# Optimization experiments

Measured on AMD Instinct MI355X. Metric: run time of the kernel, lower is better.

The kernel has to match this reference:

```python
import jax, jax.numpy as jnp
import numpy as np

B, N, E_PER_G = 32, 2048, 16384
NF, NHID, NCLS = 128, 128, 10
RATIO = 0.5
NT = B * N
E = B * E_PER_G
K1 = int(np.ceil(RATIO * N))        # 1024 nodes kept per graph after pool1
K2 = int(np.ceil(RATIO * K1))       # 512
K3 = int(np.ceil(RATIO * K2))       # 256


def setup_inputs() -> dict:
    key = jax.random.key(0)
    ks = jax.random.split(key, 16)
    x = jax.random.normal(ks[0], (NT, NF), dtype=jnp.float32)
    off = (jnp.arange(B, dtype=jnp.int32) * N)[:, None]
    src = (jax.random.randint(ks[1], (B, E_PER_G), 0, N, dtype=jnp.int32) + off).reshape(-1)
    dst = (jax.random.randint(ks[2], (B, E_PER_G), 0, N, dtype=jnp.int32) + off).reshape(-1)
    edge_index = jnp.stack([src, dst])
    batch = jnp.repeat(jnp.arange(B, dtype=jnp.int32), N)
    def lin(k, i, o):
        return jax.random.normal(k, (i, o), jnp.float32) / np.float32(np.sqrt(i))
    return {
        'x': x, 'edge_index': edge_index, 'batch': batch,
        'W1': lin(ks[3], NF, NHID), 'b1': jnp.zeros((NHID,), jnp.float32),
        'Wp1': lin(ks[4], NHID, 1), 'bp1': jnp.zeros((1,), jnp.float32),
        'W2': lin(ks[5], NHID, NHID), 'b2': jnp.zeros((NHID,), jnp.float32),
        'Wp2': lin(ks[6], NHID, 1), 'bp2': jnp.zeros((1,), jnp.float32),
        'W3': lin(ks[7], NHID, NHID), 'b3': jnp.zeros((NHID,), jnp.float32),
        'Wp3': lin(ks[8], NHID, 1), 'bp3': jnp.zeros((1,), jnp.float32),
        'lin1_W': lin(ks[9], 2 * NHID, NHID), 'lin1_b': jnp.zeros((NHID,), jnp.float32),
        'lin2_W': lin(ks[10], NHID, NHID // 2), 'lin2_b': jnp.zeros((NHID // 2,), jnp.float32),
        'lin3_W': lin(ks[11], NHID // 2, NCLS), 'lin3_b': jnp.zeros((NCLS,), jnp.float32),
    }


def gcn(x, src, dst, emask, nmask, W, b):
    # PyG GCNConv: add self-loops, symmetric normalization D^-1/2 (A+I) D^-1/2 @ (x W) + b.
    # Removed nodes/edges carry weight 0 via masks (equivalent to filter_adj re-indexing).
    h = x @ W
    deg = jnp.zeros((NT,), h.dtype).at[dst].add(emask) + nmask
    dinv = jnp.where(deg > 0, 1.0, 0.0) * jax.lax.rsqrt(jnp.where(deg > 0, deg, 1.0))
    coef = dinv[src] * dinv[dst] * emask               # [E]
    out = jnp.zeros_like(h).at[dst].add(coef[:, None] * h[src])
    out = out + ((dinv * dinv) * nmask)[:, None] * h   # self-loop term, norm = 1/deg
    return out + b


def sagpool(x, src, dst, emask, nmask, Wp, bp, k):
    # score = GCNConv(nhid,1); keep top-k per graph; x <- x[perm] * tanh(score[perm])
    score = gcn(x, src, dst, emask, nmask, Wp, bp)[:, 0]          # [NT]
    s = jnp.where(nmask > 0, score, -jnp.inf).reshape(B, N)
    _, idx = jax.lax.top_k(s, k)                                   # [B, k]
    keep = jnp.zeros((B, N), x.dtype).at[jnp.arange(B)[:, None], idx].set(1.0).reshape(-1)
    x_new = x * jnp.tanh(score)[:, None] * keep[:, None]
    emask_new = emask * keep[src] * keep[dst]                      # filter_adj
    return x_new, emask_new, keep


def readout(x, nmask, count):
    # [global_max_pool, global_mean_pool] over active nodes of each graph
    xb = x.reshape(B, N, -1)
    m = nmask.reshape(B, N, 1)
    mx = jnp.max(jnp.where(m > 0, xb, -jnp.inf), axis=1)
    mn = jnp.sum(xb * m, axis=1) / count
    return jnp.concatenate([mx, mn], axis=-1)


def reference(x, edge_index, batch, W1, b1, Wp1, bp1, W2, b2, Wp2, bp2,
              W3, b3, Wp3, bp3, lin1_W, lin1_b, lin2_W, lin2_b, lin3_W, lin3_b):
    src, dst = edge_index[0], edge_index[1]
    emask = jnp.ones((E,), x.dtype)
    nmask = jnp.ones((NT,), x.dtype)

    h = jax.nn.relu(gcn(x, src, dst, emask, nmask, W1, b1))
    h, emask, nmask = sagpool(h, src, dst, emask, nmask, Wp1, bp1, K1)
    x1 = readout(h, nmask, jnp.asarray(K1, x.dtype))

    h = jax.nn.relu(gcn(h, src, dst, emask, nmask, W2, b2))
    h, emask, nmask = sagpool(h, src, dst, emask, nmask, Wp2, bp2, K2)
    x2 = readout(h, nmask, jnp.asarray(K2, x.dtype))

    h = jax.nn.relu(gcn(h, src, dst, emask, nmask, W3, b3))
    h, emask, nmask = sagpool(h, src, dst, emask, nmask, Wp3, bp3, K3)
    x3 = readout(h, nmask, jnp.asarray(K3, x.dtype))

    g = x1 + x2 + x3
    g = jax.nn.relu(g @ lin1_W + lin1_b)   # dropout = identity in eval
    g = jax.nn.relu(g @ lin2_W + lin2_b)
    return jax.nn.log_softmax(g @ lin3_W + lin3_b, axis=-1)
```

## Files before the change

kernel.cpp:

```cpp
#include <hip/hip_runtime.h>
#include <math.h>


namespace {

constexpr int B_  = 32;
constexpr int N_  = 2048;
constexpr int NT  = B_ * N_;
constexpr int EPG = 16384;
constexpr int E_  = B_ * EPG;
constexpr int NCLS = 10;
constexpr int AST = 132;

__device__ __forceinline__ int relabel(int bpgsh) {
  int x = blockIdx.x & 7, slot = blockIdx.x >> 3;
  int g = x + 8 * (slot >> bpgsh);
  return (g << bpgsh) + (slot & ((1 << bpgsh) - 1));
}

__global__ __launch_bounds__(1024) void k_csr(const int* __restrict__ src,
                                              const int* __restrict__ dst,
                                              int* __restrict__ off,
                                              int* __restrict__ srcp,
                                              float* __restrict__ dinv,
                                              float* __restrict__ ds,
                                              float* __restrict__ sws) {
  __shared__ int hist[2048];
  __shared__ int wsum[16];
  const int g = blockIdx.x;
  const int t = threadIdx.x;
  const int base_n = g * N_;
  const int base_e = g * EPG;
  hist[t] = 0;
  hist[t + 1024] = 0;
  __syncthreads();
#pragma unroll
  for (int i = 0; i < EPG / 1024; ++i) {
    int d = dst[base_e + t + 1024 * i];
    atomicAdd(&hist[d - base_n], 1);
  }
  __syncthreads();
  int a0 = hist[2 * t], a1 = hist[2 * t + 1];
  int ps = a0 + a1;
  {
    int lane = t & 63, w = t >> 6;
    int v = ps;
#pragma unroll
    for (int o = 1; o < 64; o <<= 1) {
      int nv = __shfl_up(v, o);
      if (lane >= o) v += nv;
    }
    if (lane == 63) wsum[w] = v;
    __syncthreads();
    if (t == 0) {
      int accv = 0;
      for (int i = 0; i < 16; ++i) { int tmp = wsum[i]; wsum[i] = accv; accv += tmp; }
    }
    __syncthreads();
    int excl = wsum[w] + v - ps;
    off[base_n + 2 * t] = base_e + excl;
    off[base_n + 2 * t + 1] = base_e + excl + a0;
    hist[2 * t] = excl;
    hist[2 * t + 1] = excl + a0;
    float d0 = 1.f + (float)a0, d1 = 1.f + (float)a1;
    float di0 = 1.f / sqrtf(d0), di1 = 1.f / sqrtf(d1);
    dinv[base_n + 2 * t] = di0;
    dinv[base_n + 2 * t + 1] = di1;
    ds[base_n + 2 * t] = di0;
    ds[base_n + 2 * t + 1] = di1;
    sws[base_n + 2 * t] = di0 * di0;
    sws[base_n + 2 * t + 1] = di1 * di1;
    if (g == B_ - 1 && t == 0) off[NT] = E_;
  }
  __syncthreads();
#pragma unroll
  for (int i = 0; i < EPG / 1024; ++i) {
    int e = base_e + t + 1024 * i;
    int d = dst[e];
    int s = src[e];
    int slot = atomicAdd(&hist[d - base_n], 1);
    srcp[base_e + slot] = s;
  }
}

__global__ __launch_bounds__(256) void k_matmul(const float* __restrict__ A,
                                                const float* __restrict__ W,
                                                float* __restrict__ C,
                                                const int* __restrict__ kept,
                                                int kshift, int bpgsh,
                                                const float* __restrict__ scaleArr,
                                                float* __restrict__ pmx,
                                                float* __restrict__ psm) {
  __shared__ float Ast[2][32 * AST];
  __shared__ float Ws[2][32 * 128];
  __shared__ int rowid[128];
  __shared__ float rsc[128];
  const int tid = threadIdx.x;
  const int tile = relabel(bpgsh);
  if (kept) {
    if (tid < 128) {
      int q = tile * 128 + tid;
      int g = q >> kshift;
      int row = kept[g * N_ + (q - (g << kshift))];
      rowid[tid] = row;
      rsc[tid] = scaleArr[row];
    }
    __syncthreads();
  }
  const int rowq = tid >> 4;
  const int colq = tid & 15;
  float4 va[4], vw[4];
#pragma unroll
  for (int i = 0; i < 4; ++i) {
    int idx = tid + 256 * i;
    int row = idx & 127, fq = idx >> 7;
    int gr = kept ? rowid[row] : tile * 128 + row;
    va[i] = *(const float4*)&A[(size_t)gr * 128 + 4 * fq];
  }
#pragma unroll
  for (int i = 0; i < 4; ++i) {
    int idx = tid + 256 * i;
    int kk = idx >> 5, cf = idx & 31;
    vw[i] = *(const float4*)&W[(size_t)kk * 128 + 4 * cf];
  }
#pragma unroll
  for (int i = 0; i < 4; ++i) {
    int idx = tid + 256 * i;
    int row = idx & 127, fq = idx >> 7;
    Ast[0][(4 * fq + 0) * AST + row] = va[i].x;
    Ast[0][(4 * fq + 1) * AST + row] = va[i].y;
    Ast[0][(4 * fq + 2) * AST + row] = va[i].z;
    Ast[0][(4 * fq + 3) * AST + row] = va[i].w;
  }
#pragma unroll
  for (int i = 0; i < 4; ++i) {
    int idx = tid + 256 * i;
    int kk = idx >> 5, cf = idx & 31;
    *(float4*)&Ws[0][kk * 128 + 4 * cf] = vw[i];
  }
  __syncthreads();
  float acc[8][8] = {};
  for (int c = 0; c < 4; ++c) {
    int cur = c & 1;
    if (c < 3) {
      int k0n = 32 * (c + 1);
#pragma unroll
      for (int i = 0; i < 4; ++i) {
        int idx = tid + 256 * i;
        int row = idx & 127, fq = idx >> 7;
        int gr = kept ? rowid[row] : tile * 128 + row;
        va[i] = *(const float4*)&A[(size_t)gr * 128 + k0n + 4 * fq];
      }
#pragma unroll
      for (int i = 0; i < 4; ++i) {
        int idx = tid + 256 * i;
        int kk = idx >> 5, cf = idx & 31;
        vw[i] = *(const float4*)&W[(size_t)(k0n + kk) * 128 + 4 * cf];
      }
    }
#pragma unroll 2
    for (int kk = 0; kk < 32; ++kk) {
      float4 a0 = *(const float4*)&Ast[cur][kk * AST + 8 * rowq];
      float4 a1 = *(const float4*)&Ast[cur][kk * AST + 8 * rowq + 4];
      float4 w0 = *(const float4*)&Ws[cur][kk * 128 + 4 * colq];
      float4 w1 = *(const float4*)&Ws[cur][kk * 128 + 64 + 4 * colq];
      float a[8] = {a0.x, a0.y, a0.z, a0.w, a1.x, a1.y, a1.z, a1.w};
      float w[8] = {w0.x, w0.y, w0.z, w0.w, w1.x, w1.y, w1.z, w1.w};
#pragma unroll
      for (int r = 0; r < 8; ++r)
#pragma unroll
        for (int cc = 0; cc < 8; ++cc) acc[r][cc] += a[r] * w[cc];
    }
    if (kept) {
      int kkf = tid >> 3;
      int r0 = (tid & 7) * 16;
      float mxv = -INFINITY, smv = 0.f;
#pragma unroll
      for (int rr = 0; rr < 16; rr += 4) {
        float4 av = *(const float4*)&Ast[cur][kkf * AST + r0 + rr];
        float4 s4 = *(const float4*)&rsc[r0 + rr];
        float v0 = av.x * s4.x, v1 = av.y * s4.y;
        float v2 = av.z * s4.z, v3 = av.w * s4.w;
        mxv = fmaxf(fmaxf(fmaxf(mxv, v0), fmaxf(v1, v2)), v3);
        smv += v0 + v1 + v2 + v3;
      }
#pragma unroll
      for (int o = 4; o >= 1; o >>= 1) {
        mxv = fmaxf(mxv, __shfl_down(mxv, o));
        smv += __shfl_down(smv, o);
      }
      if ((tid & 7) == 0) {
        pmx[(size_t)tile * 128 + 32 * c + kkf] = mxv;
        psm[(size_t)tile * 128 + 32 * c + kkf] = smv;
      }
    }
    if (c < 3) {
      int nxt = cur ^ 1;
#pragma unroll
      for (int i = 0; i < 4; ++i) {
        int idx = tid + 256 * i;
        int row = idx & 127, fq = idx >> 7;
        Ast[nxt][(4 * fq + 0) * AST + row] = va[i].x;
        Ast[nxt][(4 * fq + 1) * AST + row] = va[i].y;
        Ast[nxt][(4 * fq + 2) * AST + row] = va[i].z;
        Ast[nxt][(4 * fq + 3) * AST + row] = va[i].w;
      }
#pragma unroll
      for (int i = 0; i < 4; ++i) {
        int idx = tid + 256 * i;
        int kk = idx >> 5, cf = idx & 31;
        *(float4*)&Ws[nxt][kk * 128 + 4 * cf] = vw[i];
      }
      __syncthreads();
    }
  }
#pragma unroll
  for (int r = 0; r < 8; ++r) {
    int gr = kept ? rowid[8 * rowq + r] : tile * 128 + 8 * rowq + r;
    float* Crow = &C[(size_t)gr * 128];
    *(float4*)&Crow[4 * colq] = make_float4(acc[r][0], acc[r][1], acc[r][2], acc[r][3]);
    *(float4*)&Crow[64 + 4 * colq] = make_float4(acc[r][4], acc[r][5], acc[r][6], acc[r][7]);
  }
}

__global__ __launch_bounds__(256) void k_agg(const float4* __restrict__ t4,
                                             const int* __restrict__ off,
                                             const int* __restrict__ srcp,
                                             const float* __restrict__ dinv,
                                             const float* __restrict__ ds,
                                             const float* __restrict__ sws,
                                             const float* __restrict__ bias,
                                             const float* __restrict__ Wp,
                                             float4* __restrict__ h4,
                                             float* __restrict__ t1,
                                             const int* __restrict__ kept,
                                             int kshift, int bpgsh) {
  int q = relabel(bpgsh) * 8 + (threadIdx.x >> 5);
  int node;
  if (kept) {
    int g = q >> kshift;
    node = kept[g * N_ + (q - (g << kshift))];
  } else {
    node = q;
  }
  const int lane = threadIdx.x & 31;
  const float dvi = dinv[node];
  float sw = sws[node];
  float4 self = t4[(size_t)node * 32 + lane];
  float4 acc = make_float4(sw * self.x, sw * self.y, sw * self.z, sw * self.w);
  int s = off[node], en = off[node + 1];
  int j = s;
  for (; j + 8 <= en; j += 8) {
    int sv[8];
    float cv[8];
#pragma unroll
    for (int i = 0; i < 8; ++i) sv[i] = srcp[j + i];
#pragma unroll
    for (int i = 0; i < 8; ++i) cv[i] = ds[sv[i]] * dvi;
#pragma unroll
    for (int i = 0; i < 8; ++i) {
      if (cv[i] != 0.f) {
        float4 r = t4[(size_t)sv[i] * 32 + lane];
        acc.x += cv[i] * r.x; acc.y += cv[i] * r.y;
        acc.z += cv[i] * r.z; acc.w += cv[i] * r.w;
      }
    }
  }
  for (; j < en; ++j) {
    int s0 = srcp[j];
    float c0 = ds[s0] * dvi;
    if (c0 != 0.f) {
      float4 r0 = t4[(size_t)s0 * 32 + lane];
      acc.x += c0 * r0.x; acc.y += c0 * r0.y; acc.z += c0 * r0.z; acc.w += c0 * r0.w;
    }
  }
  float4 b4 = ((const float4*)bias)[lane];
  acc.x = fmaxf(acc.x + b4.x, 0.f);
  acc.y = fmaxf(acc.y + b4.y, 0.f);
  acc.z = fmaxf(acc.z + b4.z, 0.f);
  acc.w = fmaxf(acc.w + b4.w, 0.f);
  h4[(size_t)node * 32 + lane] = acc;
  float4 wp = ((const float4*)Wp)[lane];
  float part = acc.x * wp.x + acc.y * wp.y + acc.z * wp.z + acc.w * wp.w;
#pragma unroll
  for (int o = 16; o > 0; o >>= 1) part += __shfl_down(part, o, 32);
  if (lane == 0) t1[node] = part;
}

__global__ __launch_bounds__(1024) void k_pool(const float* __restrict__ t1,
                                               const int* __restrict__ off,
                                               const int* __restrict__ srcp,
                                               float* __restrict__ dinv,
                                               float* __restrict__ ds,
                                               float* __restrict__ sws,
                                               float* __restrict__ scale,
                                               const float* __restrict__ bp,
                                               int* __restrict__ kept,
                                               const float4* __restrict__ h4,
                                               float* __restrict__ gout,
                                               float invk, int k) {
  __shared__ float st1[2048];
  __shared__ float sdv[2048];
  __shared__ float skp[2048];
  __shared__ int skept[1024];
  __shared__ unsigned rephist[4096];
  __shared__ unsigned ebits[64];
  __shared__ int wsum[16];
  __shared__ unsigned bc_digit, bc_prev;
  const int g = (blockIdx.x & 7) + 8 * (blockIdx.x >> 3);
  const int t = threadIdx.x;
  const int base = g * N_;
  st1[t] = t1[base + t];
  st1[t + 1024] = t1[base + t + 1024];
  sdv[t] = dinv[base + t];
  sdv[t + 1024] = dinv[base + t + 1024];
  if (t < 64) ebits[t] = 0u;
#pragma unroll
  for (int i = 0; i < 4; ++i) rephist[t + 1024 * i] = 0u;
  __syncthreads();
  float raw[2];
  unsigned key[2];
  float bpv = bp[0];
#pragma unroll
  for (int q = 0; q < 2; ++q) {
    int n = t + q * 1024;
    float di = sdv[n];
    float a = 0.f;
    int s = off[base + n], en = off[base + n + 1];
    int j = s;
    for (; j + 8 <= en; j += 8) {
      int sv[8];
#pragma unroll
      for (int i = 0; i < 8; ++i) sv[i] = srcp[j + i] - base;
#pragma unroll
      for (int i = 0; i < 8; ++i) a += sdv[sv[i]] * st1[sv[i]];
    }
    for (; j < en; ++j) {
      int sl = srcp[j] - base;
      a += sdv[sl] * st1[sl];
    }
    raw[q] = di * di * st1[n] + di * a + bpv;
    unsigned u = __float_as_uint(raw[q]);
    u = (u & 0x80000000u) ? ~u : (u | 0x80000000u);
    u = ~u;
    if (di <= 0.f) u = 0xFFFFFFFFu;
    key[q] = u;
  }
  unsigned prefix = 0u, rem = (unsigned)k;
  const int wv = t >> 6;
  for (int shift = 24; shift >= 0; shift -= 8) {
    unsigned mask = (shift == 24) ? 0u : (0xFFFFFFFFu << (shift + 8));
#pragma unroll
    for (int q = 0; q < 2; ++q)
      if ((key[q] & mask) == prefix)
        atomicAdd(&rephist[(wv << 8) + ((key[q] >> shift) & 255u)], 1u);
    __syncthreads();
    unsigned binv = 0u, v = 0u;
    if (t < 256) {
#pragma unroll
      for (int w = 0; w < 16; ++w) binv += rephist[(w << 8) + t];
      v = binv;
#pragma unroll
      for (int o = 1; o < 64; o <<= 1) {
        unsigned nv = __shfl_up(v, o);
        if ((t & 63) >= o) v += nv;
      }
      if ((t & 63) == 63) wsum[t >> 6] = (int)v;
    }
    __syncthreads();
    if (t < 256) {
      unsigned pre = 0u;
      int w4 = t >> 6;
      for (int u = 0; u < w4; ++u) pre += (unsigned)wsum[u];
      unsigned inc = v + pre, exc = inc - binv;
      if (inc >= rem && exc < rem) { bc_digit = (unsigned)t; bc_prev = exc; }
    }
    __syncthreads();
    if (shift > 0) {
#pragma unroll
      for (int i = 0; i < 4; ++i) rephist[t + 1024 * i] = 0u;
    }
    __syncthreads();
    prefix |= bc_digit << shift;
    rem -= bc_prev;
  }
  const unsigned Tkey = prefix;
  const int need = (int)rem;
#pragma unroll
  for (int q = 0; q < 2; ++q) {
    int n = t + q * 1024;
    if (key[q] == Tkey) atomicOr(&ebits[n >> 5], 1u << (n & 31));
  }
  __syncthreads();
#pragma unroll
  for (int q = 0; q < 2; ++q) {
    int n = t + q * 1024;
    float kp;
    if (key[q] < Tkey) {
      kp = 1.f;
    } else if (key[q] == Tkey) {
      int w = n >> 5;
      int rank = __popc(ebits[w] & ((1u << (n & 31)) - 1u));
      for (int u = 0; u < w; ++u) rank += __popc(ebits[u]);
      kp = (rank < need) ? 1.f : 0.f;
    } else {
      kp = 0.f;
    }
    skp[n] = kp;
    float sc = kp * tanhf(raw[q]);
    st1[n] = sc;
    scale[base + n] = sc;
  }
  __syncthreads();
  {
    int lane = t & 63, w = t >> 6;
    int a0 = (int)skp[2 * t], a1 = (int)skp[2 * t + 1];
    int ps = a0 + a1;
    int v = ps;
#pragma unroll
    for (int o = 1; o < 64; o <<= 1) {
      int nv = __shfl_up(v, o);
      if (lane >= o) v += nv;
    }
    if (lane == 63) wsum[w] = v;
    __syncthreads();
    if (t == 0) {
      int accv = 0;
      for (int i = 0; i < 16; ++i) { int tmp = wsum[i]; wsum[i] = accv; accv += tmp; }
    }
    __syncthreads();
    int excl = wsum[w] + v - ps;
    if (a0) { kept[base + excl] = base + 2 * t; skept[excl] = base + 2 * t; }
    if (a1) { kept[base + excl + a0] = base + 2 * t + 1; skept[excl + a0] = base + 2 * t + 1; }
  }
#pragma unroll
  for (int q = 0; q < 2; ++q) {
    int n = t + q * 1024;
    float nm = skp[n];
    float d = nm;
    int s = off[base + n], en = off[base + n + 1];
    int j = s;
    for (; j + 8 <= en; j += 8) {
      int sv[8];
#pragma unroll
      for (int i = 0; i < 8; ++i) sv[i] = srcp[j + i] - base;
#pragma unroll
      for (int i = 0; i < 8; ++i) d += skp[sv[i]];
    }
    for (; j < en; ++j) d += skp[srcp[j] - base];
    float di = (nm > 0.f) ? (1.f / sqrtf(d)) : 0.f;
    float sc = st1[n];
    dinv[base + n] = di;
    ds[base + n] = di * sc;
    sws[base + n] = di * di * sc;
  }
  if (!gout) return;
  __syncthreads();
  const int lane = t & 31, ng = t >> 5;
  float4 mx = make_float4(-INFINITY, -INFINITY, -INFINITY, -INFINITY);
  float4 sm = make_float4(0.f, 0.f, 0.f, 0.f);
  for (int i = ng; i < k; i += 32) {
    int node = skept[i];
    float sc = st1[node - base];
    float4 v = h4[(size_t)node * 32 + lane];
    v.x *= sc; v.y *= sc; v.z *= sc; v.w *= sc;
    mx.x = fmaxf(mx.x, v.x); mx.y = fmaxf(mx.y, v.y);
    mx.z = fmaxf(mx.z, v.z); mx.w = fmaxf(mx.w, v.w);
    sm.x += v.x; sm.y += v.y; sm.z += v.z; sm.w += v.w;
  }
  float4* red = (float4*)rephist;
  for (int d = 16; d >= 1; d >>= 1) {
    if (ng >= d && ng < 2 * d) {
      red[(ng - d) * 32 + lane] = mx;
      red[512 + (ng - d) * 32 + lane] = sm;
    }
    __syncthreads();
    if (ng < d) {
      float4 omx = red[ng * 32 + lane];
      float4 osm = red[512 + ng * 32 + lane];
      mx.x = fmaxf(mx.x, omx.x); mx.y = fmaxf(mx.y, omx.y);
      mx.z = fmaxf(mx.z, omx.z); mx.w = fmaxf(mx.w, omx.w);
      sm.x += osm.x; sm.y += osm.y; sm.z += osm.z; sm.w += osm.w;
    }
    __syncthreads();
  }
  if (ng == 0) {
    gout[g * 256 + 4 * lane + 0] = mx.x;
    gout[g * 256 + 4 * lane + 1] = mx.y;
    gout[g * 256 + 4 * lane + 2] = mx.z;
    gout[g * 256 + 4 * lane + 3] = mx.w;
    gout[g * 256 + 128 + 4 * lane + 0] = sm.x * invk;
    gout[g * 256 + 128 + 4 * lane + 1] = sm.y * invk;
    gout[g * 256 + 128 + 4 * lane + 2] = sm.z * invk;
    gout[g * 256 + 128 + 4 * lane + 3] = sm.w * invk;
  }
}

__global__ __launch_bounds__(128) void k_mlp(const float* __restrict__ pmxA,
                                             const float* __restrict__ psmA,
                                             const float* __restrict__ pmxB,
                                             const float* __restrict__ psmB,
                                             const float* __restrict__ goutC,
                                             const float* __restrict__ W1,
                                             const float* __restrict__ b1,
                                             const float* __restrict__ W2,
                                             const float* __restrict__ b2,
                                             const float* __restrict__ W3,
                                             const float* __restrict__ b3,
                                             float* __restrict__ out) {
  __shared__ float gr[256], o1[128], o2[64], o3[NCLS];
  int g = blockIdx.x, t = threadIdx.x;
  float mxA = -INFINITY, smA = 0.f;
#pragma unroll
  for (int p = 0; p < 8; ++p) {
    mxA = fmaxf(mxA, pmxA[(size_t)(g * 8 + p) * 128 + t]);
    smA += psmA[(size_t)(g * 8 + p) * 128 + t];
  }
  float mxB = -INFINITY, smB = 0.f;
#pragma unroll
  for (int p = 0; p < 4; ++p) {
    mxB = fmaxf(mxB, pmxB[(size_t)(g * 4 + p) * 128 + t]);
    smB += psmB[(size_t)(g * 4 + p) * 128 + t];
  }
  gr[t] = mxA + mxB + goutC[g * 256 + t];
  gr[t + 128] = smA * (1.f / 1024.f) + smB * (1.f / 512.f) + goutC[g * 256 + 128 + t];
  __syncthreads();
  float a = b1[t];
  for (int kk = 0; kk < 256; ++kk) a += gr[kk] * W1[kk * 128 + t];
  o1[t] = fmaxf(a, 0.f);
  __syncthreads();
  if (t < 64) {
    float a2 = b2[t];
    for (int kk = 0; kk < 128; ++kk) a2 += o1[kk] * W2[kk * 64 + t];
    o2[t] = fmaxf(a2, 0.f);
  }
  __syncthreads();
  if (t < NCLS) {
    float a3 = b3[t];
    for (int kk = 0; kk < 64; ++kk) a3 += o2[kk] * W3[kk * NCLS + t];
    o3[t] = a3;
  }
  __syncthreads();
  if (t == 0) {
    float m = -INFINITY;
    for (int c = 0; c < NCLS; ++c) m = fmaxf(m, o3[c]);
    float sum = 0.f;
    for (int c = 0; c < NCLS; ++c) sum += expf(o3[c] - m);
    float lse = logf(sum);
    for (int c = 0; c < NCLS; ++c) out[g * NCLS + c] = o3[c] - m - lse;
  }
}

}

extern "C" void kernel_launch(void* const* d_in, const int* in_sizes, int n_in,
                              void* d_out, int out_size, void* d_ws, size_t ws_size,
                              hipStream_t stream) {
  const float* x = (const float*)d_in[0];
  const int* ei = (const int*)d_in[1];
  const int* src = ei;
  const int* dst = ei + E_;
  const float* Wl[3]  = {(const float*)d_in[3], (const float*)d_in[7], (const float*)d_in[11]};
  const float* bl[3]  = {(const float*)d_in[4], (const float*)d_in[8], (const float*)d_in[12]};
  const float* Wpl[3] = {(const float*)d_in[5], (const float*)d_in[9], (const float*)d_in[13]};
  const float* bpl[3] = {(const float*)d_in[6], (const float*)d_in[10], (const float*)d_in[14]};
  const float* l1W = (const float*)d_in[15];
  const float* l1b = (const float*)d_in[16];
  const float* l2W = (const float*)d_in[17];
  const float* l2b = (const float*)d_in[18];
  const float* l3W = (const float*)d_in[19];
  const float* l3b = (const float*)d_in[20];

  char* p = (char*)d_ws;
  auto alloc = [&](size_t bytes) -> void* {
    void* r = (void*)p;
    p += (bytes + 255) & ~size_t(255);
    return r;
  };
  float* h      = (float*)alloc((size_t)NT * 128 * 4);
  float* t      = (float*)alloc((size_t)NT * 128 * 4);
  float* dinv   = (float*)alloc(NT * 4);
  float* ds     = (float*)alloc(NT * 4);
  float* sws    = (float*)alloc(NT * 4);
  float* scale  = (float*)alloc(NT * 4);
  float* t1     = (float*)alloc(NT * 4);
  int*   srcp   = (int*)alloc(E_ * 4);
  int*   off    = (int*)alloc((NT + 1) * 4);
  int*   kept0  = (int*)alloc(NT * 4);
  int*   kept1  = (int*)alloc(NT * 4);
  int*   kept2  = (int*)alloc(NT * 4);
  float* pmxA   = (float*)alloc(256 * 128 * 4);
  float* psmA   = (float*)alloc(256 * 128 * 4);
  float* pmxB   = (float*)alloc(128 * 128 * 4);
  float* psmB   = (float*)alloc(128 * 128 * 4);
  float* goutC  = (float*)alloc(B_ * 256 * 4);

  int* keptL[3] = {kept0, kept1, kept2};
  const int K[3] = {1024, 512, 256};
  const int KSH[3] = {10, 9, 8};
  float* pmxL[3] = {nullptr, pmxA, pmxB};
  float* psmL[3] = {nullptr, psmA, psmB};

  k_csr<<<B_, 1024, 0, stream>>>(src, dst, off, srcp, dinv, ds, sws);

  const float* inF = x;
  for (int l = 0; l < 3; ++l) {
    const int* inKept = (l == 0) ? nullptr : keptL[l - 1];
    int inKsh = (l == 0) ? 11 : KSH[l - 1];
    int nrows = (l == 0) ? NT : B_ * K[l - 1];
    int mm_bpgsh = (l == 0) ? 4 : (l == 1 ? 3 : 2);
    int ag_bpgsh = (l == 0) ? 8 : (l == 1 ? 7 : 6);
    k_matmul<<<nrows / 128, 256, 0, stream>>>(inF, Wl[l], t, inKept, inKsh, mm_bpgsh,
                                              scale, pmxL[l], psmL[l]);
    k_agg<<<nrows / 8, 256, 0, stream>>>((const float4*)t, off, srcp, dinv, ds, sws,
                                         bl[l], Wpl[l], (float4*)h, t1, inKept, inKsh,
                                         ag_bpgsh);
    k_pool<<<B_, 1024, 0, stream>>>(t1, off, srcp, dinv, ds, sws, scale, bpl[l],
                                    keptL[l], (const float4*)h,
                                    (l == 2) ? goutC : nullptr,
                                    1.f / (float)K[l], K[l]);
    inF = h;
  }
  k_mlp<<<B_, 128, 0, stream>>>(pmxA, psmA, pmxB, psmB, goutC,
                                l1W, l1b, l2W, l2b, l3W, l3b, (float*)d_out);
}
```

Measured before the change: 320.5 us.

## Fold CSR build into first matmul launch and MLP head into last pool

The CSR construction now runs in 32 extra blocks of the first matmul launch, reworked for 256-thread blocks with batched loads. The final MLP/log-softmax head is merged into the last k_pool kernel. k_pool also iterates only over the previously kept nodes instead of all 2048, and the matmul A-tile loads are remapped so consecutive threads read contiguous row segments. Together these remove two kernel launches and some redundant pool work. The costs are fewer threads for CSR building and a serial MLP tail inside the pool blocks.

```diff
diff --git a/kernel.cpp b/kernel.cpp
--- a/kernel.cpp
+++ b/kernel.cpp
@@ -12,74 +12,79 @@
 constexpr int NCLS = 10;
 constexpr int AST = 132;
 
-__device__ __forceinline__ int relabel(int bpgsh) {
-  int x = blockIdx.x & 7, slot = blockIdx.x >> 3;
+__device__ __forceinline__ int relabel(int bid, int bpgsh) {
+  int x = bid & 7, slot = bid >> 3;
   int g = x + 8 * (slot >> bpgsh);
   return (g << bpgsh) + (slot & ((1 << bpgsh) - 1));
 }
 
-__global__ __launch_bounds__(1024) void k_csr(const int* __restrict__ src,
-                                              const int* __restrict__ dst,
-                                              int* __restrict__ off,
-                                              int* __restrict__ srcp,
-                                              float* __restrict__ dinv,
-                                              float* __restrict__ ds,
-                                              float* __restrict__ sws) {
-  __shared__ int hist[2048];
-  __shared__ int wsum[16];
+__device__ void csr_build(const int* __restrict__ src, const int* __restrict__ dst,
+                          int* __restrict__ off, int* __restrict__ srcp,
+                          float* __restrict__ dinv, float* __restrict__ ds,
+                          float* __restrict__ sws, int* hist) {
   const int g = blockIdx.x;
   const int t = threadIdx.x;
   const int base_n = g * N_;
   const int base_e = g * EPG;
-  hist[t] = 0;
-  hist[t + 1024] = 0;
-  __syncthreads();
-#pragma unroll
-  for (int i = 0; i < EPG / 1024; ++i) {
-    int d = dst[base_e + t + 1024 * i];
-    atomicAdd(&hist[d - base_n], 1);
-  }
-  __syncthreads();
-  int a0 = hist[2 * t], a1 = hist[2 * t + 1];
-  int ps = a0 + a1;
+  int* wsum4 = hist + 2048;
+#pragma unroll
+  for (int i = 0; i < 8; ++i) hist[t + 256 * i] = 0;
+  __syncthreads();
+  for (int i = 0; i < EPG / 256; i += 8) {
+    int dd[8];
+#pragma unroll
+    for (int j = 0; j < 8; ++j) dd[j] = dst[base_e + t + 256 * (i + j)];
+#pragma unroll
+    for (int j = 0; j < 8; ++j) atomicAdd(&hist[dd[j] - base_n], 1);
+  }
+  __syncthreads();
+  int a[8], ssum = 0;
+#pragma unroll
+  for (int i = 0; i < 8; ++i) { a[i] = hist[8 * t + i]; ssum += a[i]; }
   {
     int lane = t & 63, w = t >> 6;
-    int v = ps;
+    int v = ssum;
 #pragma unroll
     for (int o = 1; o < 64; o <<= 1) {
       int nv = __shfl_up(v, o);
       if (lane >= o) v += nv;
     }
-    if (lane == 63) wsum[w] = v;
+    if (lane == 63) wsum4[w] = v;
     __syncthreads();
     if (t == 0) {
       int accv = 0;
-      for (int i = 0; i < 16; ++i) { int tmp = wsum[i]; wsum[i] = accv; accv += tmp; }
-    }
-    __syncthreads();
-    int excl = wsum[w] + v - ps;
-    off[base_n + 2 * t] = base_e + excl;
-    off[base_n + 2 * t + 1] = base_e + excl + a0;
-    hist[2 * t] = excl;
-    hist[2 * t + 1] = excl + a0;
-    float d0 = 1.f + (float)a0, d1 = 1.f + (float)a1;
-    float di0 = 1.f / sqrtf(d0), di1 = 1.f / sqrtf(d1);
-    dinv[base_n + 2 * t] = di0;
-    dinv[base_n + 2 * t + 1] = di1;
-    ds[base_n + 2 * t] = di0;
-    ds[base_n + 2 * t + 1] = di1;
-    sws[base_n + 2 * t] = di0 * di0;
-    sws[base_n + 2 * t + 1] = di1 * di1;
+      for (int i = 0; i < 4; ++i) { int tmp = wsum4[i]; wsum4[i] = accv; accv += tmp; }
+    }
+    __syncthreads();
+    int run = wsum4[w] + v - ssum;
+#pragma unroll
+    for (int i = 0; i < 8; ++i) {
+      int n = 8 * t + i;
+      off[base_n + n] = base_e + run;
+      hist[n] = run;
+      float d0 = 1.f + (float)a[i];
+      float di0 = 1.f / sqrtf(d0);
+      dinv[base_n + n] = di0;
+      ds[base_n + n] = di0;
+      sws[base_n + n] = di0 * di0;
+      run += a[i];
+    }
     if (g == B_ - 1 && t == 0) off[NT] = E_;
   }
   __syncthreads();
-#pragma unroll
-  for (int i = 0; i < EPG / 1024; ++i) {
-    int e = base_e + t + 1024 * i;
-    int d = dst[e];
-    int s = src[e];
-    int slot = atomicAdd(&hist[d - base_n], 1);
-    srcp[base_e + slot] = s;
+  for (int i = 0; i < EPG / 256; i += 8) {
+    int dd[8], ss[8];
+#pragma unroll
+    for (int j = 0; j < 8; ++j) {
+      int e = base_e + t + 256 * (i + j);
+      dd[j] = dst[e];
+      ss[j] = src[e];
+    }
+#pragma unroll
+    for (int j = 0; j < 8; ++j) {
+      int slot = atomicAdd(&hist[dd[j] - base_n], 1);
+      srcp[base_e + slot] = ss[j];
+    }
   }
 }
 
@@ -90,13 +95,25 @@
                                                 int kshift, int bpgsh,
                                                 const float* __restrict__ scaleArr,
                                                 float* __restrict__ pmx,
-                                                float* __restrict__ psm) {
+                                                float* __restrict__ psm,
+                                                const int* __restrict__ src,
+                                                const int* __restrict__ dst,
+                                                int* __restrict__ off,
+                                                int* __restrict__ srcp,
+                                                float* __restrict__ dinvW,
+                                                float* __restrict__ dsW,
+                                                float* __restrict__ swsW,
+                                                int csrBlocks) {
   __shared__ float Ast[2][32 * AST];
   __shared__ float Ws[2][32 * 128];
   __shared__ int rowid[128];
   __shared__ float rsc[128];
+  if ((int)blockIdx.x < csrBlocks) {
+    csr_build(src, dst, off, srcp, dinvW, dsW, swsW, (int*)&Ast[0][0]);
+    return;
+  }
   const int tid = threadIdx.x;
-  const int tile = relabel(bpgsh);
+  const int tile = relabel((int)blockIdx.x - csrBlocks, bpgsh);
   if (kept) {
     if (tid < 128) {
       int q = tile * 128 + tid;
@@ -113,9 +130,9 @@
 #pragma unroll
   for (int i = 0; i < 4; ++i) {
     int idx = tid + 256 * i;
-    int row = idx & 127, fq = idx >> 7;
-    int gr = kept ? rowid[row] : tile * 128 + row;
-    va[i] = *(const float4*)&A[(size_t)gr * 128 + 4 * fq];
+    int row = idx >> 3, f4 = idx & 7;
+    int grw = kept ? rowid[row] : tile * 128 + row;
+    va[i] = *(const float4*)&A[(size_t)grw * 128 + 4 * f4];
   }
 #pragma unroll
   for (int i = 0; i < 4; ++i) {
@@ -126,11 +143,11 @@
 #pragma unroll
   for (int i = 0; i < 4; ++i) {
     int idx = tid + 256 * i;
-    int row = idx & 127, fq = idx >> 7;
-    Ast[0][(4 * fq + 0) * AST + row] = va[i].x;
-    Ast[0][(4 * fq + 1) * AST + row] = va[i].y;
-    Ast[0][(4 * fq + 2) * AST + row] = va[i].z;
-    Ast[0][(4 * fq + 3) * AST + row] = va[i].w;
+    int row = idx >> 3, f4 = idx & 7;
+    Ast[0][(4 * f4 + 0) * AST + row] = va[i].x;
+    Ast[0][(4 * f4 + 1) * AST + row] = va[i].y;
+    Ast[0][(4 * f4 + 2) * AST + row] = va[i].z;
+    Ast[0][(4 * f4 + 3) * AST + row] = va[i].w;
   }
 #pragma unroll
   for (int i = 0; i < 4; ++i) {
@@ -147,9 +164,9 @@
 #pragma unroll
       for (int i = 0; i < 4; ++i) {
         int idx = tid + 256 * i;
-        int row = idx & 127, fq = idx >> 7;
-        int gr = kept ? rowid[row] : tile * 128 + row;
-        va[i] = *(const float4*)&A[(size_t)gr * 128 + k0n + 4 * fq];
+        int row = idx >> 3, f4 = idx & 7;
+        int grw = kept ? rowid[row] : tile * 128 + row;
+        va[i] = *(const float4*)&A[(size_t)grw * 128 + k0n + 4 * f4];
       }
 #pragma unroll
       for (int i = 0; i < 4; ++i) {
@@ -199,11 +216,11 @@
 #pragma unroll
       for (int i = 0; i < 4; ++i) {
         int idx = tid + 256 * i;
-        int row = idx & 127, fq = idx >> 7;
-        Ast[nxt][(4 * fq + 0) * AST + row] = va[i].x;
-        Ast[nxt][(4 * fq + 1) * AST + row] = va[i].y;
-        Ast[nxt][(4 * fq + 2) * AST + row] = va[i].z;
-        Ast[nxt][(4 * fq + 3) * AST + row] = va[i].w;
+        int row = idx >> 3, f4 = idx & 7;
+        Ast[nxt][(4 * f4 + 0) * AST + row] = va[i].x;
+        Ast[nxt][(4 * f4 + 1) * AST + row] = va[i].y;
+        Ast[nxt][(4 * f4 + 2) * AST + row] = va[i].z;
+        Ast[nxt][(4 * f4 + 3) * AST + row] = va[i].w;
       }
 #pragma unroll
       for (int i = 0; i < 4; ++i) {
@@ -216,8 +233,8 @@
   }
 #pragma unroll
   for (int r = 0; r < 8; ++r) {
-    int gr = kept ? rowid[8 * rowq + r] : tile * 128 + 8 * rowq + r;
-    float* Crow = &C[(size_t)gr * 128];
+    int grw = kept ? rowid[8 * rowq + r] : tile * 128 + 8 * rowq + r;
+    float* Crow = &C[(size_t)grw * 128];
     *(float4*)&Crow[4 * colq] = make_float4(acc[r][0], acc[r][1], acc[r][2], acc[r][3]);
     *(float4*)&Crow[64 + 4 * colq] = make_float4(acc[r][4], acc[r][5], acc[r][6], acc[r][7]);
   }
@@ -235,7 +252,7 @@
                                              float* __restrict__ t1,
                                              const int* __restrict__ kept,
                                              int kshift, int bpgsh) {
-  int q = relabel(bpgsh) * 8 + (threadIdx.x >> 5);
+  int q = relabel(blockIdx.x, bpgsh) * 8 + (threadIdx.x >> 5);
   int node;
   if (kept) {
     int g = q >> kshift;
@@ -297,8 +314,19 @@
                                                const float* __restrict__ bp,
                                                int* __restrict__ kept,
                                                const float4* __restrict__ h4,
-                                               float* __restrict__ gout,
-                                               float invk, int k) {
+                                               float invk, int k,
+                                               const int* __restrict__ inKept, int klen,
+                                               const float* __restrict__ pmxA,
+                                               const float* __restrict__ psmA,
+                                               const float* __restrict__ pmxB,
+                                               const float* __restrict__ psmB,
+                                               const float* __restrict__ hW1,
+                                               const float* __restrict__ hb1,
+                                               const float* __restrict__ hW2,
+                                               const float* __restrict__ hb2,
+                                               const float* __restrict__ hW3,
+                                               const float* __restrict__ hb3,
+                                               float* __restrict__ out) {
   __shared__ float st1[2048];
   __shared__ float sdv[2048];
   __shared__ float skp[2048];
@@ -307,6 +335,7 @@
   __shared__ unsigned ebits[64];
   __shared__ int wsum[16];
   __shared__ unsigned bc_digit, bc_prev;
+  __shared__ float gr[256], o1[128], o2[64], o3[NCLS];
   const int g = (blockIdx.x & 7) + 8 * (blockIdx.x >> 3);
   const int t = threadIdx.x;
   const int base = g * N_;
@@ -314,16 +343,22 @@
   st1[t + 1024] = t1[base + t + 1024];
   sdv[t] = dinv[base + t];
   sdv[t + 1024] = dinv[base + t + 1024];
+  skp[t] = 0.f;
+  skp[t + 1024] = 0.f;
   if (t < 64) ebits[t] = 0u;
 #pragma unroll
   for (int i = 0; i < 4; ++i) rephist[t + 1024 * i] = 0u;
   __syncthreads();
-  float raw[2];
-  unsigned key[2];
+  int nodeq[2] = {-1, -1};
+  float raw[2] = {0.f, 0.f};
+  unsigned key[2] = {0xFFFFFFFFu, 0xFFFFFFFFu};
   float bpv = bp[0];
 #pragma unroll
   for (int q = 0; q < 2; ++q) {
-    int n = t + q * 1024;
+    int i = t + q * 1024;
+    if (i >= klen) continue;
+    int n = inKept ? (inKept[base + i] - base) : i;
+    nodeq[q] = n;
     float di = sdv[n];
     float a = 0.f;
     int s = off[base + n], en = off[base + n + 1];
@@ -331,9 +366,9 @@
     for (; j + 8 <= en; j += 8) {
       int sv[8];
 #pragma unroll
-      for (int i = 0; i < 8; ++i) sv[i] = srcp[j + i] - base;
-#pragma unroll
-      for (int i = 0; i < 8; ++i) a += sdv[sv[i]] * st1[sv[i]];
+      for (int i2 = 0; i2 < 8; ++i2) sv[i2] = srcp[j + i2] - base;
+#pragma unroll
+      for (int i2 = 0; i2 < 8; ++i2) a += sdv[sv[i2]] * st1[sv[i2]];
     }
     for (; j < en; ++j) {
       int sl = srcp[j] - base;
@@ -352,7 +387,7 @@
     unsigned mask = (shift == 24) ? 0u : (0xFFFFFFFFu << (shift + 8));
 #pragma unroll
     for (int q = 0; q < 2; ++q)
-      if ((key[q] & mask) == prefix)
+      if (nodeq[q] >= 0 && (key[q] & mask) == prefix)
         atomicAdd(&rephist[(wv << 8) + ((key[q] >> shift) & 255u)], 1u);
     __syncthreads();
     unsigned binv = 0u, v = 0u;
@@ -388,13 +423,14 @@
   const int need = (int)rem;
 #pragma unroll
   for (int q = 0; q < 2; ++q) {
-    int n = t + q * 1024;
-    if (key[q] == Tkey) atomicOr(&ebits[n >> 5], 1u << (n & 31));
+    int n = nodeq[q];
+    if (n >= 0 && key[q] == Tkey) atomicOr(&ebits[n >> 5], 1u << (n & 31));
   }
   __syncthreads();
 #pragma unroll
   for (int q = 0; q < 2; ++q) {
-    int n = t + q * 1024;
+    int n = nodeq[q];
+    if (n < 0) continue;
     float kp;
     if (key[q] < Tkey) {
       kp = 1.f;
@@ -435,7 +471,8 @@
   }
 #pragma unroll
   for (int q = 0; q < 2; ++q) {
-    int n = t + q * 1024;
+    int n = nodeq[q];
+    if (n < 0) continue;
     float nm = skp[n];
     float d = nm;
     int s = off[base + n], en = off[base + n + 1];
@@ -443,9 +480,9 @@
     for (; j + 8 <= en; j += 8) {
       int sv[8];
 #pragma unroll
-      for (int i = 0; i < 8; ++i) sv[i] = srcp[j + i] - base;
-#pragma unroll
-      for (int i = 0; i < 8; ++i) d += skp[sv[i]];
+      for (int i2 = 0; i2 < 8; ++i2) sv[i2] = srcp[j + i2] - base;
+#pragma unroll
+      for (int i2 = 0; i2 < 8; ++i2) d += skp[sv[i2]];
     }
     for (; j < en; ++j) d += skp[srcp[j] - base];
     float di = (nm > 0.f) ? (1.f / sqrtf(d)) : 0.f;
@@ -454,7 +491,7 @@
     ds[base + n] = di * sc;
     sws[base + n] = di * di * sc;
   }
-  if (!gout) return;
+  if (!out) return;
   __syncthreads();
   const int lane = t & 31, ng = t >> 5;
   float4 mx = make_float4(-INFINITY, -INFINITY, -INFINITY, -INFINITY);
@@ -485,59 +522,48 @@
     __syncthreads();
   }
   if (ng == 0) {
-    gout[g * 256 + 4 * lane + 0] = mx.x;
-    gout[g * 256 + 4 * lane + 1] = mx.y;
-    gout[g * 256 + 4 * lane + 2] = mx.z;
-    gout[g * 256 + 4 * lane + 3] = mx.w;
-    gout[g * 256 + 128 + 4 * lane + 0] = sm.x * invk;
-    gout[g * 256 + 128 + 4 * lane + 1] = sm.y * invk;
-    gout[g * 256 + 128 + 4 * lane + 2] = sm.z * invk;
-    gout[g * 256 + 128 + 4 * lane + 3] = sm.w * invk;
-  }
-}
-
-__global__ __launch_bounds__(128) void k_mlp(const float* __restrict__ pmxA,
-                                             const float* __restrict__ psmA,
-                                             const float* __restrict__ pmxB,
-                                             const float* __restrict__ psmB,
-                                             const float* __restrict__ goutC,
-                                             const float* __restrict__ W1,
-                                             const float* __restrict__ b1,
-                                             const float* __restrict__ W2,
-                                             const float* __restrict__ b2,
-                                             const float* __restrict__ W3,
-                                             const float* __restrict__ b3,
-                                             float* __restrict__ out) {
-  __shared__ float gr[256], o1[128], o2[64], o3[NCLS];
-  int g = blockIdx.x, t = threadIdx.x;
-  float mxA = -INFINITY, smA = 0.f;
-#pragma unroll
-  for (int p = 0; p < 8; ++p) {
-    mxA = fmaxf(mxA, pmxA[(size_t)(g * 8 + p) * 128 + t]);
-    smA += psmA[(size_t)(g * 8 + p) * 128 + t];
-  }
-  float mxB = -INFINITY, smB = 0.f;
-#pragma unroll
-  for (int p = 0; p < 4; ++p) {
-    mxB = fmaxf(mxB, pmxB[(size_t)(g * 4 + p) * 128 + t]);
-    smB += psmB[(size_t)(g * 4 + p) * 128 + t];
-  }
-  gr[t] = mxA + mxB + goutC[g * 256 + t];
-  gr[t + 128] = smA * (1.f / 1024.f) + smB * (1.f / 512.f) + goutC[g * 256 + 128 + t];
-  __syncthreads();
-  float a = b1[t];
-  for (int kk = 0; kk < 256; ++kk) a += gr[kk] * W1[kk * 128 + t];
-  o1[t] = fmaxf(a, 0.f);
+    gr[4 * lane + 0] = mx.x;
+    gr[4 * lane + 1] = mx.y;
+    gr[4 * lane + 2] = mx.z;
+    gr[4 * lane + 3] = mx.w;
+    gr[128 + 4 * lane + 0] = sm.x * invk;
+    gr[128 + 4 * lane + 1] = sm.y * invk;
+    gr[128 + 4 * lane + 2] = sm.z * invk;
+    gr[128 + 4 * lane + 3] = sm.w * invk;
+  }
+  __syncthreads();
+  if (t < 128) {
+    float mxA = -INFINITY, smA = 0.f;
+#pragma unroll
+    for (int p = 0; p < 8; ++p) {
+      mxA = fmaxf(mxA, pmxA[(size_t)(g * 8 + p) * 128 + t]);
+      smA += psmA[(size_t)(g * 8 + p) * 128 + t];
+    }
+    float mxB = -INFINITY, smB = 0.f;
+#pragma unroll
+    for (int p = 0; p < 4; ++p) {
+      mxB = fmaxf(mxB, pmxB[(size_t)(g * 4 + p) * 128 + t]);
+      smB += psmB[(size_t)(g * 4 + p) * 128 + t];
+    }
+    gr[t] += mxA + mxB;
+    gr[t + 128] += smA * (1.f / 1024.f) + smB * (1.f / 512.f);
+  }
+  __syncthreads();
+  if (t < 128) {
+    float a = hb1[t];
+    for (int kk = 0; kk < 256; ++kk) a += gr[kk] * hW1[kk * 128 + t];
+    o1[t] = fmaxf(a, 0.f);
+  }
   __syncthreads();
   if (t < 64) {
-    float a2 = b2[t];
-    for (int kk = 0; kk < 128; ++kk) a2 += o1[kk] * W2[kk * 64 + t];
+    float a2 = hb2[t];
+    for (int kk = 0; kk < 128; ++kk) a2 += o1[kk] * hW2[kk * 64 + t];
     o2[t] = fmaxf(a2, 0.f);
   }
   __syncthreads();
   if (t < NCLS) {
-    float a3 = b3[t];
-    for (int kk = 0; kk < 64; ++kk) a3 += o2[kk] * W3[kk * NCLS + t];
+    float a3 = hb3[t];
+    for (int kk = 0; kk < 64; ++kk) a3 += o2[kk] * hW3[kk * NCLS + t];
     o3[t] = a3;
   }
   __syncthreads();
@@ -593,15 +619,12 @@
   float* psmA   = (float*)alloc(256 * 128 * 4);
   float* pmxB   = (float*)alloc(128 * 128 * 4);
   float* psmB   = (float*)alloc(128 * 128 * 4);
-  float* goutC  = (float*)alloc(B_ * 256 * 4);
 
   int* keptL[3] = {kept0, kept1, kept2};
   const int K[3] = {1024, 512, 256};
   const int KSH[3] = {10, 9, 8};
   float* pmxL[3] = {nullptr, pmxA, pmxB};
   float* psmL[3] = {nullptr, psmA, psmB};
-
-  k_csr<<<B_, 1024, 0, stream>>>(src, dst, off, srcp, dinv, ds, sws);
 
   const float* inF = x;
   for (int l = 0; l < 3; ++l) {
@@ -610,17 +633,22 @@
     int nrows = (l == 0) ? NT : B_ * K[l - 1];
     int mm_bpgsh = (l == 0) ? 4 : (l == 1 ? 3 : 2);
     int ag_bpgsh = (l == 0) ? 8 : (l == 1 ? 7 : 6);
-    k_matmul<<<nrows / 128, 256, 0, stream>>>(inF, Wl[l], t, inKept, inKsh, mm_bpgsh,
-                                              scale, pmxL[l], psmL[l]);
+    int csrB = (l == 0) ? B_ : 0;
+    int klen = (l == 0) ? N_ : K[l - 1];
+    bool last = (l == 2);
+    k_matmul<<<nrows / 128 + csrB, 256, 0, stream>>>(
+        inF, Wl[l], t, inKept, inKsh, mm_bpgsh, scale, pmxL[l], psmL[l],
+        src, dst, off, srcp, dinv, ds, sws, csrB);
     k_agg<<<nrows / 8, 256, 0, stream>>>((const float4*)t, off, srcp, dinv, ds, sws,
                                          bl[l], Wpl[l], (float4*)h, t1, inKept, inKsh,
                                          ag_bpgsh);
     k_pool<<<B_, 1024, 0, stream>>>(t1, off, srcp, dinv, ds, sws, scale, bpl[l],
                                     keptL[l], (const float4*)h,
-                                    (l == 2) ? goutC : nullptr,
-                                    1.f / (float)K[l], K[l]);
+                                    1.f / (float)K[l], K[l], inKept, klen,
+                                    last ? pmxA : nullptr, last ? psmA : nullptr,
+                                    last ? pmxB : nullptr, last ? psmB : nullptr,
+                                    l1W, l1b, l2W, l2b, l3W, l3b,
+                                    last ? (float*)d_out : nullptr);
     inF = h;
   }
-  k_mlp<<<B_, 128, 0, stream>>>(pmxA, psmA, pmxB, psmB, goutC,
-                                l1W, l1b, l2W, l2b, l3W, l3b, (float*)d_out);
 }
```

Result: faster. 299.1 us (-6.7%).
